# Optimization experiments

Hardware: AMD Instinct MI355X
Metric: run time of the kernel (lower is better)

Reference implementation:

```python
import math
import jax, jax.numpy as jnp
import numpy as np

B = 8
NUM_POINTS = 4096
LATENT = 512
HID = 512
AD = 128
R1, R2, R_ATT = 1.0, 1.5, 0.2
EPS = 1e-5
SQRT_D = math.sqrt(AD)


def _fibonacci_sphere_points(n, radius):
    if n <= 0:
        return np.zeros((0, 3), np.float32)
    i = np.arange(n, dtype=np.float32)
    phi = (1 + 5 ** 0.5) / 2
    theta = 2 * math.pi * i / phi
    z = 1.0 - 2.0 * (i + 0.5) / n
    r_xy = np.sqrt(np.maximum(1.0 - z * z, 0.0))
    return (radius * np.stack((r_xy * np.cos(theta), r_xy * np.sin(theta), z), axis=-1)).astype(np.float32)


def _make_template():
    n_shell = NUM_POINTS - 1
    area_ratio = R1 ** 2 / (R1 ** 2 + R2 ** 2)
    n1 = max(1, round(n_shell * area_ratio))
    n2 = n_shell - n1
    if n2 == 0:
        n1, n2 = n1 - 1, 1
    t1 = _fibonacci_sphere_points(n1, R1)
    t2 = _fibonacci_sphere_points(n2, R2)
    return jnp.asarray(np.concatenate([np.zeros((1, 3), np.float32), t1, t2], axis=0))


def setup_inputs() -> dict:
    key = jax.random.key(0)
    ks = iter(jax.random.split(key, 64))
    d = {}
    d['z'] = jax.random.normal(next(ks), (B, LATENT), jnp.float32)
    d['template'] = _make_template()
    d['wq'] = jax.random.normal(next(ks), (AD, 3), jnp.float32) * 0.1
    d['wk'] = jax.random.normal(next(ks), (AD, 3), jnp.float32) * 0.1
    d['wv'] = jax.random.normal(next(ks), (AD, 3), jnp.float32) * 0.1
    in_dims = [LATENT + 3, LATENT + 3 + AD, LATENT + 3 + AD]
    for s, in_dim in enumerate(in_dims):
        d[f's{s}_w1'] = jax.random.normal(next(ks), (HID, in_dim), jnp.float32) * (1.0 / math.sqrt(in_dim))
        d[f's{s}_b1'] = jnp.zeros((HID,), jnp.float32)
        d[f's{s}_g1'] = jnp.ones((HID,), jnp.float32)
        d[f's{s}_be1'] = jnp.zeros((HID,), jnp.float32)
        d[f's{s}_w2'] = jax.random.normal(next(ks), (HID, HID), jnp.float32) * (1.0 / math.sqrt(HID))
        d[f's{s}_b2'] = jnp.zeros((HID,), jnp.float32)
        d[f's{s}_g2'] = jnp.ones((HID,), jnp.float32)
        d[f's{s}_be2'] = jnp.zeros((HID,), jnp.float32)
        d[f's{s}_w3'] = jax.random.normal(next(ks), (3, HID), jnp.float32) * (1.0 / math.sqrt(HID))
        d[f's{s}_b3'] = jnp.zeros((3,), jnp.float32)
    return d


def _bn_relu(x, gamma, beta):
    # BatchNorm1d in training mode over channel dim of (B, N, C): stats over (B, N)
    mean = jnp.mean(x, axis=(0, 1))
    var = jnp.var(x, axis=(0, 1))
    xn = (x - mean) * jax.lax.rsqrt(var + EPS)
    return jax.nn.relu(xn * gamma + beta)


def _stage(x, w1, b1, g1, be1, w2, b2, g2, be2, w3, b3):
    h = _bn_relu(x @ w1.T + b1, g1, be1)
    h = _bn_relu(h @ w2.T + b2, g2, be2)
    return h @ w3.T + b3


def _local_attention(coords, wq, wk, wv):
    Q = coords @ wq.T  # (B, N, AD)
    K = coords @ wk.T
    V = coords @ wv.T
    sq = jnp.sum(coords * coords, axis=-1)  # (B, N)
    D2 = sq[:, :, None] + sq[:, None, :] - 2.0 * jnp.einsum('bnd,bmd->bnm', coords, coords)
    mask = D2 <= R_ATT ** 2  # diagonal always True (D2=0)
    scores = jnp.einsum('bnd,bmd->bnm', Q, K) / SQRT_D
    scores = jnp.where(mask, scores, -jnp.inf)
    W = jax.nn.softmax(scores, axis=-1)
    W = jnp.where(mask, W, 0.0)
    return jnp.einsum('bnm,bmd->bnd', W, V)


def reference(z, template, wq, wk, wv,
              s0_w1, s0_b1, s0_g1, s0_be1, s0_w2, s0_b2, s0_g2, s0_be2, s0_w3, s0_b3,
              s1_w1, s1_b1, s1_g1, s1_be1, s1_w2, s1_b2, s1_g2, s1_be2, s1_w3, s1_b3,
              s2_w1, s2_b1, s2_g1, s2_be1, s2_w2, s2_b2, s2_g2, s2_be2, s2_w3, s2_b3):
    Bz = z.shape[0]
    z_exp = jnp.broadcast_to(z[:, None, :], (Bz, NUM_POINTS, LATENT))
    tmpl = jnp.broadcast_to(template[None], (Bz, NUM_POINTS, 3))
    coords0 = _stage(jnp.concatenate((z_exp, tmpl), axis=-1),
                     s0_w1, s0_b1, s0_g1, s0_be1, s0_w2, s0_b2, s0_g2, s0_be2, s0_w3, s0_b3)
    attn1 = _local_attention(coords0, wq, wk, wv)
    coords1 = _stage(jnp.concatenate((z_exp, coords0, attn1), axis=-1),
                     s1_w1, s1_b1, s1_g1, s1_be1, s1_w2, s1_b2, s1_g2, s1_be2, s1_w3, s1_b3)
    attn2 = _local_attention(coords1, wq, wk, wv)
    coords2 = _stage(jnp.concatenate((z_exp, coords1, attn2), axis=-1),
                     s2_w1, s2_b1, s2_g1, s2_be1, s2_w2, s2_b2, s2_g2, s2_be2, s2_w3, s2_b3)
    return coords2
```

## Files before the change

### kernel.cpp

```cpp
#include <hip/hip_runtime.h>
#include <math.h>

#define NPTS 4096
#define BATCH 8
#define HIDD 512
#define ROWS 32768
#define R_ATT2 0.04f
#define INV_SQRT_D 0.08838834764831845f
#define LOG2E 1.4426950408889634f

typedef unsigned short u16;
typedef unsigned int u32;
typedef __attribute__((ext_vector_type(8))) short s8v;
typedef __attribute__((ext_vector_type(4))) float f4v;
typedef __attribute__((ext_vector_type(4))) u32 u4v;

__device__ __forceinline__ float u2f(u16 v) { return __uint_as_float(((u32)v) << 16); }
__device__ __forceinline__ u16 f2u(float f) {
  u32 u = __float_as_uint(f);
  return (u16)((u + 0x7fffu + ((u >> 16) & 1u)) >> 16);
}
__device__ __forceinline__ u32 packtrunc(float x0, float x1) {
  return (__float_as_uint(x1) & 0xFFFF0000u) | (__float_as_uint(x0) >> 16);
}
__device__ __forceinline__ float fast_exp2(float x) {
  float r;
  asm("v_exp_f32 %0, %1" : "=v"(r) : "v"(x));
  return r;
}
__device__ __forceinline__ s8v mk8(u32 a, u32 b, u32 c, u32 d) {
  union { u4v u; s8v s; } x;
  x.u = (u4v){a, b, c, d};
  return x.s;
}

__global__ void gram_k(const float* __restrict__ wq, const float* __restrict__ wk,
                       float* __restrict__ G) {
  int ab = threadIdx.x;
  if (ab < 9) {
    int a = ab / 3, b = ab % 3;
    float s = 0.f;
    for (int d = 0; d < 128; ++d) s = fmaf(wq[d * 3 + a], wk[d * 3 + b], s);
    G[ab] = s;
  }
}

__global__ __launch_bounds__(256) void prep2_k(
    const float* __restrict__ z, const float* __restrict__ w1, int ldw,
    const float* __restrict__ b1, const float* __restrict__ w2,
    float* __restrict__ zwbuf, float* __restrict__ ubuf,
    u16* __restrict__ w1abf, u16* __restrict__ w2bf, int doW1a) {
  int wid = blockIdx.x * 4 + (threadIdx.x >> 6);
  int lane = threadIdx.x & 63;
  {
    int b = wid >> 9, c = wid & 511;
    const float* zr = z + b * 512;
    const float* wr = w1 + (size_t)c * ldw;
    float acc = 0.f;
#pragma unroll
    for (int k = lane; k < 512; k += 64) acc = fmaf(zr[k], wr[k], acc);
#pragma unroll
    for (int off = 32; off; off >>= 1) acc += __shfl_down(acc, off);
    if (lane == 0) zwbuf[wid] = acc + b1[c];
  }
  int idx = blockIdx.x * 256 + threadIdx.x;
  if (idx < 1536) {
    int a = idx >> 9, c = idx & 511;
    ubuf[idx] = w1[(size_t)c * ldw + 512 + a];
  }
  if (doW1a && idx < 65536) {
    int n = idx >> 7, k = idx & 127;
    w1abf[idx] = f2u(w1[(size_t)n * 643 + 515 + k]);
  }
  w2bf[idx] = f2u(w2[idx]);
}

__global__ __launch_bounds__(256) void s0l1s_k(const float* __restrict__ tmpl,
                                               const float* __restrict__ u,
                                               const float* __restrict__ zw,
                                               u16* __restrict__ h,
                                               float* __restrict__ psum,
                                               float* __restrict__ psumsq) {
  __shared__ float Ls[4][512];
  __shared__ float Lq[4][512];
  int g = blockIdx.x;
  int wave = threadIdx.x >> 6, lane = threadIdx.x & 63;
  int b = g >> 8;
  int c0 = lane * 8;
  const float* zr = zw + b * 512 + c0;
  const float* u0 = u + c0;
  const float* u1 = u + 512 + c0;
  const float* u2 = u + 1024 + c0;
  float zv[8], u0v[8], u1v[8], u2v[8];
#pragma unroll
  for (int j = 0; j < 8; ++j) {
    zv[j] = zr[j]; u0v[j] = u0[j]; u1v[j] = u1[j]; u2v[j] = u2[j];
  }
  float s[8] = {0, 0, 0, 0, 0, 0, 0, 0}, q[8] = {0, 0, 0, 0, 0, 0, 0, 0};
  int row0 = g * 16 + wave * 4;
#pragma unroll
  for (int t = 0; t < 4; ++t) {
    int row = row0 + t;
    int n = row & (NPTS - 1);
    float tx = tmpl[n * 3], ty = tmpl[n * 3 + 1], tz = tmpl[n * 3 + 2];
    u32 outw[4];
#pragma unroll
    for (int jj = 0; jj < 4; ++jj) {
      float v0 = zv[2 * jj] + tx * u0v[2 * jj] + ty * u1v[2 * jj] + tz * u2v[2 * jj];
      float v1 = zv[2 * jj + 1] + tx * u0v[2 * jj + 1] + ty * u1v[2 * jj + 1] + tz * u2v[2 * jj + 1];
      outw[jj] = packtrunc(v0, v1);
      float r0 = u2f((u16)(outw[jj] & 0xffffu));
      float r1 = u2f((u16)(outw[jj] >> 16));
      s[2 * jj] += r0;     q[2 * jj] = fmaf(r0, r0, q[2 * jj]);
      s[2 * jj + 1] += r1; q[2 * jj + 1] = fmaf(r1, r1, q[2 * jj + 1]);
    }
    *(uint4*)(h + (size_t)row * 512 + c0) = *(const uint4*)outw;
  }
#pragma unroll
  for (int j = 0; j < 8; ++j) {
    Ls[wave][c0 + j] = s[j];
    Lq[wave][c0 + j] = q[j];
  }
  __syncthreads();
  int c2 = threadIdx.x * 2;
#pragma unroll
  for (int cc = 0; cc < 2; ++cc) {
    int c = c2 + cc;
    psum[g * 512 + c] = Ls[0][c] + Ls[1][c] + Ls[2][c] + Ls[3][c];
    psumsq[g * 512 + c] = Lq[0][c] + Lq[1][c] + Lq[2][c] + Lq[3][c];
  }
}

__global__ __launch_bounds__(256) void bnrelu_k(u16* __restrict__ h,
                                                const float* __restrict__ sc,
                                                const float* __restrict__ sh) {
  int nthreads = gridDim.x * 256;
  int total = ROWS * 512 / 8;
  for (int i = blockIdx.x * 256 + threadIdx.x; i < total; i += nthreads) {
    int k0 = (i * 8) & 511;
    uint4 v = *(const uint4*)(h + (size_t)i * 8);
    const u16* p = (const u16*)&v;
    u32 outw[4];
#pragma unroll
    for (int t = 0; t < 4; ++t) {
      float x0 = fmaxf(fmaf(u2f(p[2 * t]), sc[k0 + 2 * t], sh[k0 + 2 * t]), 0.f);
      float x1 = fmaxf(fmaf(u2f(p[2 * t + 1]), sc[k0 + 2 * t + 1], sh[k0 + 2 * t + 1]), 0.f);
      outw[t] = packtrunc(x0, x1);
    }
    *(uint4*)(h + (size_t)i * 8) = *(const uint4*)outw;
  }
}

template <bool MODE1>
__global__ __launch_bounds__(256) void gemm_mfma_k(
    const u16* __restrict__ A, int lda, const u16* __restrict__ B, int ldb, int K,
    const float* __restrict__ bias, const float* __restrict__ zw,
    const float* __restrict__ u, const float4* __restrict__ c4,
    u16* __restrict__ C, float* __restrict__ psum, float* __restrict__ psumsq) {
  __shared__ u16 As[128 * 32];
  __shared__ u16 Bs[128 * 32];
  int tid = threadIdx.x;
  int wave = tid >> 6, lane = tid & 63;
  int quad = lane >> 4, l16 = lane & 15;
  int m0 = blockIdx.x * 128, n0 = blockIdx.y * 128;
  int wm = (wave & 1) * 64, wn = (wave >> 1) * 64;
  int srow0 = lane >> 2;
  int sc8 = (lane & 3) * 8;
  f4v acc[4][4];
#pragma unroll
  for (int mi = 0; mi < 4; ++mi)
#pragma unroll
    for (int ni = 0; ni < 4; ++ni) acc[mi][ni] = (f4v){0.f, 0.f, 0.f, 0.f};

  for (int k0 = 0; k0 < K; k0 += 32) {
#pragma unroll
    for (int j = 0; j < 2; ++j) {
      int chunk = wave * 2 + j;
      int row = chunk * 16 + srow0;
      const u16* gA = A + (size_t)(m0 + row) * lda + k0 + sc8;
      const u16* gB = B + (size_t)(n0 + row) * ldb + k0 + sc8;
      __builtin_amdgcn_global_load_lds(
          (const __attribute__((address_space(1))) void*)gA,
          (__attribute__((address_space(3))) void*)(As + chunk * 512), 16, 0, 0);
      __builtin_amdgcn_global_load_lds(
          (const __attribute__((address_space(1))) void*)gB,
          (__attribute__((address_space(3))) void*)(Bs + chunk * 512), 16, 0, 0);
    }
    __syncthreads();
    s8v af[4], bfv[4];
#pragma unroll
    for (int mi = 0; mi < 4; ++mi)
      af[mi] = *(const s8v*)&As[(wm + mi * 16 + l16) * 32 + quad * 8];
#pragma unroll
    for (int ni = 0; ni < 4; ++ni)
      bfv[ni] = *(const s8v*)&Bs[(wn + ni * 16 + l16) * 32 + quad * 8];
#pragma unroll
    for (int mi = 0; mi < 4; ++mi)
#pragma unroll
      for (int ni = 0; ni < 4; ++ni)
        acc[mi][ni] = __builtin_amdgcn_mfma_f32_16x16x32_bf16(
            af[mi], bfv[ni], acc[mi][ni], 0, 0, 0);
    __syncthreads();
  }

  int batch = m0 >> 12;
  float e0[4], e1[4], e2[4], e3[4];
  float ps[4] = {0, 0, 0, 0}, pq[4] = {0, 0, 0, 0};
#pragma unroll
  for (int ni = 0; ni < 4; ++ni) {
    int gn = n0 + wn + ni * 16 + l16;
    if (MODE1) {
      e0[ni] = zw[batch * 512 + gn];
      e1[ni] = u[gn];
      e2[ni] = u[512 + gn];
      e3[ni] = u[1024 + gn];
    } else {
      e0[ni] = bias[gn];
    }
  }
#pragma unroll
  for (int mi = 0; mi < 4; ++mi) {
#pragma unroll
    for (int reg = 0; reg < 4; ++reg) {
      int gm = m0 + wm + mi * 16 + quad * 4 + reg;
      float cx = 0.f, cy = 0.f, cz = 0.f;
      if (MODE1) {
        float4 p = c4[gm];
        cx = p.x; cy = p.y; cz = p.z;
      }
#pragma unroll
      for (int ni = 0; ni < 4; ++ni) {
        int gn = n0 + wn + ni * 16 + l16;
        float v = acc[mi][ni][reg] + e0[ni];
        if (MODE1) v += cx * e1[ni] + cy * e2[ni] + cz * e3[ni];
        u16 r = f2u(v);
        C[(size_t)gm * 512 + gn] = r;
        float vr = u2f(r);
        ps[ni] += vr;
        pq[ni] = fmaf(vr, vr, pq[ni]);
      }
    }
  }
  float* Lps = (float*)As;
  float* Lpq = (float*)Bs;
#pragma unroll
  for (int ni = 0; ni < 4; ++ni) {
    Lps[((wave * 4 + quad) * 4 + ni) * 16 + l16] = ps[ni];
    Lpq[((wave * 4 + quad) * 4 + ni) * 16 + l16] = pq[ni];
  }
  __syncthreads();
  if (tid < 128) {
    int wn2 = tid >> 6, rem = tid & 63;
    int nni = rem >> 4, ll = rem & 15;
    int gn = n0 + wn2 * 64 + nni * 16 + ll;
    float s = 0.f, q = 0.f;
#pragma unroll
    for (int wv = 0; wv < 2; ++wv)
#pragma unroll
      for (int qd = 0; qd < 4; ++qd) {
        int w2 = wn2 * 2 + wv;
        s += Lps[((w2 * 4 + qd) * 4 + nni) * 16 + ll];
        q += Lpq[((w2 * 4 + qd) * 4 + nni) * 16 + ll];
      }
    psum[(size_t)blockIdx.x * 512 + gn] = s;
    psumsq[(size_t)blockIdx.x * 512 + gn] = q;
  }
}

__global__ __launch_bounds__(256) void bn_fin_k(
    const float* __restrict__ psum, const float* __restrict__ psumsq, int nslabs,
    const float* __restrict__ gamma, const float* __restrict__ beta,
    float* __restrict__ sc, float* __restrict__ sh) {
  int c = blockIdx.x * 4 + (threadIdx.x >> 6);
  int lane = threadIdx.x & 63;
  float s = 0.f, q = 0.f;
  for (int g = lane; g < nslabs; g += 64) {
    s += psum[g * 512 + c];
    q += psumsq[g * 512 + c];
  }
#pragma unroll
  for (int off = 32; off; off >>= 1) {
    s += __shfl_down(s, off);
    q += __shfl_down(q, off);
  }
  if (lane == 0) {
    float mean = s * (1.f / 32768.f);
    float var = fmaxf(q * (1.f / 32768.f) - mean * mean, 0.f);
    float inv = rsqrtf(var + 1e-5f);
    float scale = gamma[c] * inv;
    sc[c] = scale;
    sh[c] = beta[c] - mean * scale;
  }
}

__global__ __launch_bounds__(256) void l3_k(const u16* __restrict__ h,
                                            const float* __restrict__ sc,
                                            const float* __restrict__ sh,
                                            const float* __restrict__ w3,
                                            const float* __restrict__ b3,
                                            float4* __restrict__ c4out,
                                            float* __restrict__ fout) {
  int wid = blockIdx.x * 4 + (threadIdx.x >> 6);
  int lane = threadIdx.x & 63;
  int k0 = lane * 8;
  uint4 hv = *(const uint4*)(h + (size_t)wid * 512 + k0);
  const u16* hp = (const u16*)&hv;
  float a0 = 0, a1 = 0, a2 = 0;
#pragma unroll
  for (int j = 0; j < 8; ++j) {
    int k = k0 + j;
    float x = fmaxf(fmaf(u2f(hp[j]), sc[k], sh[k]), 0.f);
    a0 = fmaf(x, w3[k], a0);
    a1 = fmaf(x, w3[512 + k], a1);
    a2 = fmaf(x, w3[1024 + k], a2);
  }
#pragma unroll
  for (int off = 32; off; off >>= 1) {
    a0 += __shfl_down(a0, off);
    a1 += __shfl_down(a1, off);
    a2 += __shfl_down(a2, off);
  }
  if (lane == 0) {
    a0 += b3[0]; a1 += b3[1]; a2 += b3[2];
    if (c4out) {
      float sq = a0 * a0 + a1 * a1 + a2 * a2;
      c4out[wid] = make_float4(a0, a1, a2, sq);
    }
    if (fout) {
      fout[(size_t)wid * 3 + 0] = a0;
      fout[(size_t)wid * 3 + 1] = a1;
      fout[(size_t)wid * 3 + 2] = a2;
    }
  }
}

__global__ __launch_bounds__(512) void attnm_k(const float4* __restrict__ c4,
                                               const float* __restrict__ G,
                                               const float* __restrict__ wv,
                                               u16* __restrict__ attnb) {
  __shared__ __align__(16) char lds[65536 + 4096 + 8192];
  int wave = threadIdx.x >> 6, lane = threadIdx.x & 63;
  int g = lane >> 4, q16 = lane & 15;
  int qbase = blockIdx.x * 64;
  int b = qbase >> 12;
  const float4* cb = c4 + (size_t)b * NPTS;
  int pt0 = wave * 512;
  char* ebufW = lds + wave * 8192;
  char* ctW = lds + 65536 + wave * 512;
  float* fin = (float*)(lds + 65536 + 4096);

  float Gr[9];
#pragma unroll
  for (int i = 0; i < 9; ++i) Gr[i] = G[i];
  u32 bh0[4], bh1[4], bh2[4], bh3[4];
  u32 sh0[4], sh1[4], sh2[4], sh3[4];
  float thr[4];
#pragma unroll
  for (int s = 0; s < 4; ++s) {
    float4 cq = c4[qbase + s * 16 + q16];
    thr[s] = 0.5f * (cq.w - R_ATT2);
    u16 hx = f2u(cq.x), hy = f2u(cq.y), hz = f2u(cq.z);
    u16 lx = f2u(cq.x - u2f(hx)), ly = f2u(cq.y - u2f(hy)), lz = f2u(cq.z - u2f(hz));
    u32 h01 = (u32)hx | ((u32)hy << 16);
    u32 h23 = (u32)hz | (0x3F80u << 16);
    u32 l01 = (u32)lx | ((u32)ly << 16);
    u32 l23 = (u32)lz;
    bh0[s] = (g <= 1) ? h01 : 0u;
    bh1[s] = (g <= 1) ? h23 : 0u;
    bh2[s] = (g == 0) ? l01 : 0u;
    bh3[s] = (g == 0) ? l23 : 0u;
    const float SC = INV_SQRT_D * LOG2E;
    float g0v = (cq.x * Gr[0] + cq.y * Gr[3] + cq.z * Gr[6]) * SC;
    float g1v = (cq.x * Gr[1] + cq.y * Gr[4] + cq.z * Gr[7]) * SC;
    float g2v = (cq.x * Gr[2] + cq.y * Gr[5] + cq.z * Gr[8]) * SC;
    u16 ghx = f2u(g0v), ghy = f2u(g1v), ghz = f2u(g2v);
    u16 glx = f2u(g0v - u2f(ghx)), gly = f2u(g1v - u2f(ghy)), glz = f2u(g2v - u2f(ghz));
    u32 gh01 = (u32)ghx | ((u32)ghy << 16);
    u32 gh23 = (u32)ghz;
    u32 gl01 = (u32)glx | ((u32)gly << 16);
    u32 gl23 = (u32)glz;
    sh0[s] = (g <= 1) ? gh01 : 0u;
    sh1[s] = (g <= 1) ? gh23 : 0u;
    sh2[s] = (g == 0) ? gl01 : 0u;
    sh3[s] = (g == 0) ? gl23 : 0u;
  }

  f4v pvAcc[4];
#pragma unroll
  for (int s = 0; s < 4; ++s) pvAcc[s] = (f4v){0.f, 0.f, 0.f, 0.f};

  for (int w = 0; w < 16; ++w) {
    int wpar = w & 1;
    char* ebuf = ebufW + wpar * 4096;
    char* ct = ctW + wpar * 256;
#pragma unroll
    for (int tp = 0; tp < 2; ++tp) {
      int p = pt0 + w * 32 + tp * 16 + q16;
      float4 pp = cb[p];
      float nhw = -0.5f * pp.w;
      u16 hx = f2u(pp.x), hy = f2u(pp.y), hz = f2u(pp.z), hw = f2u(nhw);
      u16 lx = f2u(pp.x - u2f(hx)), ly = f2u(pp.y - u2f(hy));
      u16 lz = f2u(pp.z - u2f(hz)), lw = f2u(nhw - u2f(hw));
      u32 h01 = (u32)hx | ((u32)hy << 16), h23 = (u32)hz | ((u32)hw << 16);
      u32 l01 = (u32)lx | ((u32)ly << 16), l23 = (u32)lz | ((u32)lw << 16);
      u32 a0 = (g == 0) ? h01 : ((g == 1) ? l01 : 0u);
      u32 a1 = (g == 0) ? h23 : ((g == 1) ? l23 : 0u);
      u32 a2 = (g == 0) ? h01 : 0u;
      u32 a3 = (g == 0) ? h23 : 0u;
      s8v av = mk8(a0, a1, a2, a3);
      if (g == 0) {
        *(u16*)(ct + 64 + tp * 32 + q16 * 2) = hx;
        *(u16*)(ct + 128 + tp * 32 + q16 * 2) = hy;
        *(u16*)(ct + 192 + tp * 32 + q16 * 2) = hz;
      }
#pragma unroll
      for (int s = 0; s < 4; ++s) {
        f4v z4 = (f4v){0.f, 0.f, 0.f, 0.f};
        f4v dmv = __builtin_amdgcn_mfma_f32_16x16x32_bf16(
            av, mk8(bh0[s], bh1[s], bh2[s], bh3[s]), z4, 0, 0, 0);
        f4v s2v = __builtin_amdgcn_mfma_f32_16x16x32_bf16(
            av, mk8(sh0[s], sh1[s], sh2[s], sh3[s]), z4, 0, 0, 0);
        float e0 = (dmv[0] >= thr[s]) ? fast_exp2(s2v[0]) : 0.f;
        float e1 = (dmv[1] >= thr[s]) ? fast_exp2(s2v[1]) : 0.f;
        float e2 = (dmv[2] >= thr[s]) ? fast_exp2(s2v[2]) : 0.f;
        float e3 = (dmv[3] >= thr[s]) ? fast_exp2(s2v[3]) : 0.f;
        u32* ew = (u32*)(ebuf + s * 1024 + q16 * 64 + tp * 32 + g * 8);
        ew[0] = (u32)f2u(e0) | ((u32)f2u(e1) << 16);
        ew[1] = (u32)f2u(e2) | ((u32)f2u(e3) << 16);
      }
    }
    int cc = q16 & 3;
    u4v bt = *(const u4v*)(ct + cc * 64 + g * 16);
    if (q16 == 0) bt = (u4v){0x3F803F80u, 0x3F803F80u, 0x3F803F80u, 0x3F803F80u};
    s8v pvB = mk8(bt.x, bt.y, bt.z, bt.w);
#pragma unroll
    for (int s = 0; s < 4; ++s) {
      u4v at = *(const u4v*)(ebuf + s * 1024 + q16 * 64 + g * 16);
      pvAcc[s] = __builtin_amdgcn_mfma_f32_16x16x32_bf16(
          mk8(at.x, at.y, at.z, at.w), pvB, pvAcc[s], 0, 0, 0);
    }
  }

  if (q16 < 4) {
#pragma unroll
    for (int s = 0; s < 4; ++s)
#pragma unroll
      for (int r = 0; r < 4; ++r)
        fin[wave * 256 + (s * 16 + g * 4 + r) * 4 + q16] = pvAcc[s][r];
  }
  __syncthreads();
  float* comb = (float*)lds;
  int t = threadIdx.x;
  if (t < 256) {
    int qb = t >> 2, c = t & 3;
    float acc = 0.f;
#pragma unroll
    for (int wv8 = 0; wv8 < 8; ++wv8) acc += fin[wv8 * 256 + qb * 4 + c];
    comb[qb * 4 + c] = acc;
  }
  __syncthreads();
#pragma unroll
  for (int it = 0; it < 8; ++it) {
    int task = t + it * 512;
    int qb = task >> 6, dp = task & 63;
    float sw = comb[qb * 4 + 0];
    float sx = comb[qb * 4 + 1];
    float sy = comb[qb * 4 + 2];
    float sz = comb[qb * 4 + 3];
    float inv = 1.f / sw;
    float ox = sx * inv, oy = sy * inv, oz = sz * inv;
    int d0 = dp * 2;
    float v0 = ox * wv[d0 * 3] + oy * wv[d0 * 3 + 1] + oz * wv[d0 * 3 + 2];
    float v1 = ox * wv[d0 * 3 + 3] + oy * wv[d0 * 3 + 4] + oz * wv[d0 * 3 + 5];
    u32 pack = (u32)f2u(v0) | ((u32)f2u(v1) << 16);
    *(u32*)(attnb + (size_t)(qbase + qb) * 128 + d0) = pack;
  }
}

extern "C" void kernel_launch(void* const* d_in, const int* in_sizes, int n_in,
                              void* d_out, int out_size, void* d_ws, size_t ws_size,
                              hipStream_t stream) {
  const float* z = (const float*)d_in[0];
  const float* tmpl = (const float*)d_in[1];
  const float* wq = (const float*)d_in[2];
  const float* wk = (const float*)d_in[3];
  const float* wv = (const float*)d_in[4];
  const float* sw[3][10];
  for (int s = 0; s < 3; ++s)
    for (int j = 0; j < 10; ++j) sw[s][j] = (const float*)d_in[5 + s * 10 + j];

  char* base = (char*)d_ws;
  size_t off = 0;
  auto alloc = [&](size_t bytes) -> void* {
    void* p = base + off;
    off = (off + bytes + 255) & ~(size_t)255;
    return p;
  };
  u16* hA = (u16*)alloc((size_t)ROWS * 512 * 2);
  u16* hB = (u16*)alloc((size_t)ROWS * 512 * 2);
  u16* attnb = (u16*)alloc((size_t)ROWS * 128 * 2);
  float4* c4 = (float4*)alloc((size_t)ROWS * 16);
  float* psum = (float*)alloc(2048 * 512 * 4);
  float* psumsq = (float*)alloc(2048 * 512 * 4);
  float* zwbuf = (float*)alloc(4096 * 4);
  float* scv = (float*)alloc(512 * 4);
  float* shv = (float*)alloc(512 * 4);
  float* G = (float*)alloc(256);
  u16* w1abf = (u16*)alloc(512 * 128 * 2);
  u16* w2bf = (u16*)alloc(512 * 512 * 2);
  float* ubuf = (float*)alloc(1536 * 4);

  gram_k<<<1, 64, 0, stream>>>(wq, wk, G);

  for (int s = 0; s < 3; ++s) {
    int ldw = (s == 0) ? 515 : 643;
    prep2_k<<<1024, 256, 0, stream>>>(z, sw[s][0], ldw, sw[s][1], sw[s][4],
                                      zwbuf, ubuf, w1abf, w2bf, s == 0 ? 0 : 1);
    if (s == 0) {
      s0l1s_k<<<2048, 256, 0, stream>>>(tmpl, ubuf, zwbuf, hA, psum, psumsq);
      bn_fin_k<<<128, 256, 0, stream>>>(psum, psumsq, 2048,
                                        sw[s][2], sw[s][3], scv, shv);
    } else {
      gemm_mfma_k<true><<<dim3(256, 4), 256, 0, stream>>>(
          attnb, 128, w1abf, 128, 128, nullptr, zwbuf, ubuf, c4,
          hA, psum, psumsq);
      bn_fin_k<<<128, 256, 0, stream>>>(psum, psumsq, 256,
                                        sw[s][2], sw[s][3], scv, shv);
    }
    bnrelu_k<<<2048, 256, 0, stream>>>(hA, scv, shv);
    gemm_mfma_k<false><<<dim3(256, 4), 256, 0, stream>>>(
        hA, 512, w2bf, 512, 512, sw[s][5], nullptr, nullptr, nullptr,
        hB, psum, psumsq);
    bn_fin_k<<<128, 256, 0, stream>>>(psum, psumsq, 256,
                                      sw[s][6], sw[s][7], scv, shv);
    bool last = (s == 2);
    l3_k<<<8192, 256, 0, stream>>>(hB, scv, shv, sw[s][8], sw[s][9],
                                   last ? nullptr : c4,
                                   last ? (float*)d_out : nullptr);
    if (!last) {
      attnm_k<<<512, 512, 0, stream>>>(c4, G, wv, attnb);
    }
  }
}
```

Measured before the change: 492.4 us.

## Precompute key bf16 split fragments in a prep kernel and swizzle LDS exp buffer

Adds a small cprep_k kernel that converts every point's coordinates into hi/lo bf16 MFMA fragments and a transposed coordinate tile once. The attention kernel then loads these directly instead of redoing the split for each query block, which removes per-block conversion work and the LDS staging of coordinate tiles. It also XOR-swizzles the exp-weight LDS layout to reduce bank conflicts, and switches to truncating bf16 packing of the exp values. The cost is an extra launch, more global memory traffic, and slightly less accurate rounding of the weights.

```diff
diff --git a/kernel.cpp b/kernel.cpp
--- a/kernel.cpp
+++ b/kernel.cpp
@@ -14,6 +14,7 @@
 typedef __attribute__((ext_vector_type(8))) short s8v;
 typedef __attribute__((ext_vector_type(4))) float f4v;
 typedef __attribute__((ext_vector_type(4))) u32 u4v;
+typedef __attribute__((ext_vector_type(2))) u32 u2v;
 
 __device__ __forceinline__ float u2f(u16 v) { return __uint_as_float(((u32)v) << 16); }
 __device__ __forceinline__ u16 f2u(float f) {
@@ -334,20 +335,41 @@
   }
 }
 
+__global__ __launch_bounds__(256) void cprep_k(const float4* __restrict__ c4,
+                                               u4v* __restrict__ frag,
+                                               u16* __restrict__ ctg) {
+  int i = blockIdx.x * 256 + threadIdx.x;
+  float4 p = c4[i];
+  float nhw = -0.5f * p.w;
+  u16 hx = f2u(p.x), hy = f2u(p.y), hz = f2u(p.z), hw = f2u(nhw);
+  u16 lx = f2u(p.x - u2f(hx)), ly = f2u(p.y - u2f(hy));
+  u16 lz = f2u(p.z - u2f(hz)), lw = f2u(nhw - u2f(hw));
+  u32 h01 = (u32)hx | ((u32)hy << 16), h23 = (u32)hz | ((u32)hw << 16);
+  u32 l01 = (u32)lx | ((u32)ly << 16), l23 = (u32)lz | ((u32)lw << 16);
+  frag[i] = (u4v){h01, h23, l01, l23};
+  int chunk = i >> 5, p32 = i & 31;
+  u16* base = ctg + (size_t)chunk * 128;
+  base[p32] = 0x3F80;
+  base[32 + p32] = hx;
+  base[64 + p32] = hy;
+  base[96 + p32] = hz;
+}
+
 __global__ __launch_bounds__(512) void attnm_k(const float4* __restrict__ c4,
+                                               const u4v* __restrict__ frag,
+                                               const u16* __restrict__ ctg,
                                                const float* __restrict__ G,
                                                const float* __restrict__ wv,
                                                u16* __restrict__ attnb) {
-  __shared__ __align__(16) char lds[65536 + 4096 + 8192];
+  __shared__ __align__(16) char lds[65536 + 8192];
   int wave = threadIdx.x >> 6, lane = threadIdx.x & 63;
   int g = lane >> 4, q16 = lane & 15;
   int qbase = blockIdx.x * 64;
   int b = qbase >> 12;
-  const float4* cb = c4 + (size_t)b * NPTS;
   int pt0 = wave * 512;
   char* ebufW = lds + wave * 8192;
-  char* ctW = lds + 65536 + wave * 512;
-  float* fin = (float*)(lds + 65536 + 4096);
+  float* fin = (float*)(lds + 65536);
+  int chunk0 = b * 128 + (pt0 >> 5);
 
   float Gr[9];
 #pragma unroll
@@ -389,30 +411,19 @@
 #pragma unroll
   for (int s = 0; s < 4; ++s) pvAcc[s] = (f4v){0.f, 0.f, 0.f, 0.f};
 
+  int csw = g ^ (q16 & 3);
   for (int w = 0; w < 16; ++w) {
-    int wpar = w & 1;
-    char* ebuf = ebufW + wpar * 4096;
-    char* ct = ctW + wpar * 256;
+    char* ebuf = ebufW + (w & 1) * 4096;
 #pragma unroll
     for (int tp = 0; tp < 2; ++tp) {
       int p = pt0 + w * 32 + tp * 16 + q16;
-      float4 pp = cb[p];
-      float nhw = -0.5f * pp.w;
-      u16 hx = f2u(pp.x), hy = f2u(pp.y), hz = f2u(pp.z), hw = f2u(nhw);
-      u16 lx = f2u(pp.x - u2f(hx)), ly = f2u(pp.y - u2f(hy));
-      u16 lz = f2u(pp.z - u2f(hz)), lw = f2u(nhw - u2f(hw));
-      u32 h01 = (u32)hx | ((u32)hy << 16), h23 = (u32)hz | ((u32)hw << 16);
-      u32 l01 = (u32)lx | ((u32)ly << 16), l23 = (u32)lz | ((u32)lw << 16);
-      u32 a0 = (g == 0) ? h01 : ((g == 1) ? l01 : 0u);
-      u32 a1 = (g == 0) ? h23 : ((g == 1) ? l23 : 0u);
-      u32 a2 = (g == 0) ? h01 : 0u;
-      u32 a3 = (g == 0) ? h23 : 0u;
+      u4v f = frag[(size_t)b * NPTS + p];
+      u32 a0 = (g == 0) ? f.x : ((g == 1) ? f.z : 0u);
+      u32 a1 = (g == 0) ? f.y : ((g == 1) ? f.w : 0u);
+      u32 a2 = (g == 0) ? f.x : 0u;
+      u32 a3 = (g == 0) ? f.y : 0u;
       s8v av = mk8(a0, a1, a2, a3);
-      if (g == 0) {
-        *(u16*)(ct + 64 + tp * 32 + q16 * 2) = hx;
-        *(u16*)(ct + 128 + tp * 32 + q16 * 2) = hy;
-        *(u16*)(ct + 192 + tp * 32 + q16 * 2) = hz;
-      }
+      int wsw = ((tp * 2 + (g >> 1)) ^ (q16 & 3)) * 16 + (g & 1) * 8;
 #pragma unroll
       for (int s = 0; s < 4; ++s) {
         f4v z4 = (f4v){0.f, 0.f, 0.f, 0.f};
@@ -424,18 +435,16 @@
         float e1 = (dmv[1] >= thr[s]) ? fast_exp2(s2v[1]) : 0.f;
         float e2 = (dmv[2] >= thr[s]) ? fast_exp2(s2v[2]) : 0.f;
         float e3 = (dmv[3] >= thr[s]) ? fast_exp2(s2v[3]) : 0.f;
-        u32* ew = (u32*)(ebuf + s * 1024 + q16 * 64 + tp * 32 + g * 8);
-        ew[0] = (u32)f2u(e0) | ((u32)f2u(e1) << 16);
-        ew[1] = (u32)f2u(e2) | ((u32)f2u(e3) << 16);
+        u2v ew = (u2v){packtrunc(e0, e1), packtrunc(e2, e3)};
+        *(u2v*)(ebuf + s * 1024 + q16 * 64 + wsw) = ew;
       }
     }
-    int cc = q16 & 3;
-    u4v bt = *(const u4v*)(ct + cc * 64 + g * 16);
-    if (q16 == 0) bt = (u4v){0x3F803F80u, 0x3F803F80u, 0x3F803F80u, 0x3F803F80u};
+    const u16* ctb = ctg + (size_t)(chunk0 + w) * 128 + (q16 & 3) * 32 + g * 8;
+    u4v bt = *(const u4v*)ctb;
     s8v pvB = mk8(bt.x, bt.y, bt.z, bt.w);
 #pragma unroll
     for (int s = 0; s < 4; ++s) {
-      u4v at = *(const u4v*)(ebuf + s * 1024 + q16 * 64 + g * 16);
+      u4v at = *(const u4v*)(ebuf + s * 1024 + q16 * 64 + csw * 16);
       pvAcc[s] = __builtin_amdgcn_mfma_f32_16x16x32_bf16(
           mk8(at.x, at.y, at.z, at.w), pvB, pvAcc[s], 0, 0, 0);
     }
@@ -509,6 +518,8 @@
   u16* w1abf = (u16*)alloc(512 * 128 * 2);
   u16* w2bf = (u16*)alloc(512 * 512 * 2);
   float* ubuf = (float*)alloc(1536 * 4);
+  u4v* fragb = (u4v*)alloc((size_t)ROWS * 16);
+  u16* ctg = (u16*)alloc((size_t)1024 * 128 * 2);
 
   gram_k<<<1, 64, 0, stream>>>(wq, wk, G);
 
@@ -538,7 +549,8 @@
                                    last ? nullptr : c4,
                                    last ? (float*)d_out : nullptr);
     if (!last) {
-      attnm_k<<<512, 512, 0, stream>>>(c4, G, wv, attnb);
-    }
-  }
-}
+      cprep_k<<<128, 256, 0, stream>>>(c4, fragb, ctg);
+      attnm_k<<<512, 512, 0, stream>>>(c4, fragb, ctg, G, wv, attnb);
+    }
+  }
+}
```

New measurement: 466.7 us. 1.06x faster.
